# Kernel optimization log

Measured on AMD Instinct MI355X. Metric: run time of the kernel, lower is better.

Reference implementation:

```python
import jax, jax.numpy as jnp
import numpy as np

NUM_CLUSTERS = 32
EPS = 1e-12

def _l2norm(v, axis):
    return v / jnp.maximum(jnp.linalg.norm(v, axis=axis, keepdims=True), EPS)

def setup_inputs() -> dict:
    key = jax.random.key(0)
    k1, k2, k3 = jax.random.split(key, 3)
    B, M, D, K = 64, 512, 2048, NUM_CLUSTERS
    init_sc = 1.0 / np.sqrt(D)
    x = jax.random.normal(k1, (B, M, D), dtype=jnp.float32)
    W = init_sc * jax.random.normal(k2, (K, D), dtype=jnp.float32)
    centroids = init_sc * jax.random.normal(k3, (K, D), dtype=jnp.float32)
    return {"x": x, "W": W, "centroids": centroids}

def reference(x, W, centroids):
    # x: [B, M, D] frame features; W: [K, D]; centroids: [K, D]
    xn = _l2norm(x, axis=-1)                              # per-frame L2 normalize
    sa = jax.nn.softmax(jnp.einsum('bmd,kd->bmk', xn, W), axis=-1)  # [B, M, K]
    # vlad[b,k,d] = sum_m sa[b,m,k] * (xn[b,m,d] - centroids[k,d])
    #            = (sa^T @ xn)[b,k,d] - colsum(sa)[b,k] * centroids[k,d]
    agg = jnp.einsum('bmk,bmd->bkd', sa, xn)              # [B, K, D]
    vlad = agg - jnp.sum(sa, axis=1)[..., None] * centroids[None]
    vlad = _l2norm(vlad, axis=2)                          # intra-normalize per cluster
    vlad = vlad.reshape(vlad.shape[0], -1)                # [B, K*D]
    return _l2norm(vlad, axis=1)
```

## Files before the change

### kernel.cpp

```cpp
#include <hip/hip_runtime.h>
#include <hip/hip_bf16.h>
#include <cstdint>
#include <cstddef>

#define Bn 64
#define Mn 512
#define Dn 2048
#define Kn 32
#define EPSF 1e-12f

typedef __attribute__((ext_vector_type(8))) __bf16 bf16x8;
typedef __attribute__((ext_vector_type(4))) __bf16 bf16x4;
typedef __attribute__((ext_vector_type(4))) float f32x4;

__global__ __launch_bounds__(256) void k0_prep(const float* __restrict__ W,
                                               __bf16* __restrict__ Wb,
                                               float* __restrict__ colsum,
                                               float* __restrict__ ssq) {
  int idx = blockIdx.x * 256 + threadIdx.x;
  if (idx < Kn * Dn) Wb[idx] = (__bf16)W[idx];
  if (idx < Bn * Kn) { colsum[idx] = 0.f; ssq[idx] = 0.f; }
}

__global__ __launch_bounds__(256) void k1_logits_softmax(const float* __restrict__ x,
                                                         const __bf16* __restrict__ Wb,
                                                         __bf16* __restrict__ saT,
                                                         float* __restrict__ colsum) {
  int wv = threadIdx.x >> 6, lane = threadIdx.x & 63;
  int mr = lane & 15, q = lane >> 4;
  int row0 = (blockIdx.x * 4 + wv) * 16;
  int b = row0 >> 9;
  const float* xp = x + (size_t)(row0 + mr) * Dn + q * 8;
  const __bf16* wp = Wb + (size_t)mr * Dn + q * 8;
  f32x4 acc0 = {0.f, 0.f, 0.f, 0.f};
  f32x4 acc1 = {0.f, 0.f, 0.f, 0.f};
  float ssq = 0.f;
#pragma unroll 2
  for (int s = 0; s < 64; ++s) {
    f32x4 xa = *(const f32x4*)(xp + s * 32);
    f32x4 xb = *(const f32x4*)(xp + s * 32 + 4);
    bf16x8 af;
    af[0] = (__bf16)xa[0]; af[1] = (__bf16)xa[1];
    af[2] = (__bf16)xa[2]; af[3] = (__bf16)xa[3];
    af[4] = (__bf16)xb[0]; af[5] = (__bf16)xb[1];
    af[6] = (__bf16)xb[2]; af[7] = (__bf16)xb[3];
    ssq = fmaf(xa[0], xa[0], ssq); ssq = fmaf(xa[1], xa[1], ssq);
    ssq = fmaf(xa[2], xa[2], ssq); ssq = fmaf(xa[3], xa[3], ssq);
    ssq = fmaf(xb[0], xb[0], ssq); ssq = fmaf(xb[1], xb[1], ssq);
    ssq = fmaf(xb[2], xb[2], ssq); ssq = fmaf(xb[3], xb[3], ssq);
    bf16x8 b0 = *(const bf16x8*)(wp + s * 32);
    bf16x8 b1 = *(const bf16x8*)(wp + (size_t)16 * Dn + s * 32);
    acc0 = __builtin_amdgcn_mfma_f32_16x16x32_bf16(af, b0, acc0, 0, 0, 0);
    acc1 = __builtin_amdgcn_mfma_f32_16x16x32_bf16(af, b1, acc1, 0, 0, 0);
  }
  ssq += __shfl_xor(ssq, 16);
  ssq += __shfl_xor(ssq, 32);
  float invb = 1.f / fmaxf(sqrtf(ssq), EPSF);
  float cs0 = 0.f, cs1 = 0.f;
  bf16x4 v40, v41;
#pragma unroll
  for (int r = 0; r < 4; ++r) {
    float inv = __shfl(invb, q * 4 + r);
    float v0 = acc0[r] * inv, v1 = acc1[r] * inv;
    float mx = fmaxf(v0, v1);
    mx = fmaxf(mx, __shfl_xor(mx, 1));
    mx = fmaxf(mx, __shfl_xor(mx, 2));
    mx = fmaxf(mx, __shfl_xor(mx, 4));
    mx = fmaxf(mx, __shfl_xor(mx, 8));
    float e0 = __expf(v0 - mx), e1 = __expf(v1 - mx);
    float sm = e0 + e1;
    sm += __shfl_xor(sm, 1); sm += __shfl_xor(sm, 2);
    sm += __shfl_xor(sm, 4); sm += __shfl_xor(sm, 8);
    float rs = 1.f / sm;
    float sa0 = e0 * rs, sa1 = e1 * rs;
    v40[r] = (__bf16)(sa0 * inv);
    v41[r] = (__bf16)(sa1 * inv);
    cs0 += sa0; cs1 += sa1;
  }
  int mloc = row0 & 511;
  __bf16* st = saT + ((size_t)(b * Kn + mr)) * Mn + mloc + q * 4;
  *(bf16x4*)st = v40;
  *(bf16x4*)(st + (size_t)16 * Mn) = v41;
  cs0 += __shfl_xor(cs0, 16); cs0 += __shfl_xor(cs0, 32);
  cs1 += __shfl_xor(cs1, 16); cs1 += __shfl_xor(cs1, 32);
  if (lane < 16) {
    atomicAdd(&colsum[b * Kn + mr], cs0);
    atomicAdd(&colsum[b * Kn + mr + 16], cs1);
  }
}

#define AS 520
__global__ __launch_bounds__(256) void k3_agg(const float* __restrict__ x,
                                              const __bf16* __restrict__ saT,
                                              const float* __restrict__ colsum,
                                              const float* __restrict__ cent,
                                              float* __restrict__ vlad,
                                              float* __restrict__ ssq) {
  __shared__ __bf16 sal[Kn * AS];
  __shared__ float csl[Kn];
  int b = blockIdx.x >> 4;
  int dchunk = (blockIdx.x & 15) * 128;
  int t = threadIdx.x;
  const __bf16* sg = saT + (size_t)b * Kn * Mn;
#pragma unroll
  for (int i = 0; i < 8; ++i) {
    int u = t + 256 * i;
    int kr = u >> 6, off = (u & 63) * 8;
    *(bf16x8*)&sal[kr * AS + off] = *(const bf16x8*)(sg + (size_t)kr * Mn + off);
  }
  if (t < Kn) csl[t] = colsum[b * Kn + t];
  __syncthreads();
  int w = t >> 6, lane = t & 63;
  int n = lane & 15, q = lane >> 4;
  int d0 = dchunk + w * 32;
  const float* xg = x + (size_t)b * Mn * Dn;
  f32x4 acc[2][2] = {};
  for (int m0 = 0; m0 < Mn; m0 += 32) {
    bf16x8 a0 = *(const bf16x8*)&sal[n * AS + m0 + q * 8];
    bf16x8 a1 = *(const bf16x8*)&sal[(n + 16) * AS + m0 + q * 8];
#pragma unroll
    for (int dt = 0; dt < 2; ++dt) {
      const float* xp = xg + (size_t)(m0 + q * 8) * Dn + d0 + dt * 16 + n;
      bf16x8 bv;
#pragma unroll
      for (int j = 0; j < 8; ++j) bv[j] = (__bf16)xp[(size_t)j * Dn];
      acc[dt][0] = __builtin_amdgcn_mfma_f32_16x16x32_bf16(a0, bv, acc[dt][0], 0, 0, 0);
      acc[dt][1] = __builtin_amdgcn_mfma_f32_16x16x32_bf16(a1, bv, acc[dt][1], 0, 0, 0);
    }
  }
#pragma unroll
  for (int dt = 0; dt < 2; ++dt) {
#pragma unroll
    for (int kt = 0; kt < 2; ++kt) {
#pragma unroll
      for (int r = 0; r < 4; ++r) {
        int k = kt * 16 + q * 4 + r;
        int d = d0 + dt * 16 + n;
        float vv = acc[dt][kt][r] - csl[k] * cent[(size_t)k * Dn + d];
        vlad[((size_t)(b * Kn + k)) * Dn + d] = vv;
        float sq = vv * vv;
        sq += __shfl_xor(sq, 1); sq += __shfl_xor(sq, 2);
        sq += __shfl_xor(sq, 4); sq += __shfl_xor(sq, 8);
        if (n == 0) atomicAdd(&ssq[b * Kn + k], sq);
      }
    }
  }
}

__global__ __launch_bounds__(256) void k4_norm(float* __restrict__ out,
                                               const float* __restrict__ ssq) {
  __shared__ float rk[Kn];
  __shared__ float us[Kn];
  int b = blockIdx.x >> 4;
  int t = threadIdx.x;
  if (t < Kn) {
    float ss = ssq[b * Kn + t];
    float r = 1.f / fmaxf(sqrtf(ss), EPSF);
    rk[t] = r;
    us[t] = ss * r * r;
  }
  __syncthreads();
  float S = 0.f;
#pragma unroll
  for (int k = 0; k < Kn; ++k) S += us[k];
  float s = 1.f / fmaxf(sqrtf(S), EPSF);
  int chunk = blockIdx.x & 15;
  size_t base = (size_t)b * (Kn * Dn) + (size_t)chunk * 4096;
  f32x4* p = (f32x4*)(out + base);
#pragma unroll
  for (int i = 0; i < 4; ++i) {
    int idx = t + 256 * i;
    int k = (chunk * 4096 + idx * 4) >> 11;
    f32x4 v = p[idx];
    float sc = rk[k] * s;
    v[0] *= sc; v[1] *= sc; v[2] *= sc; v[3] *= sc;
    p[idx] = v;
  }
}

extern "C" void kernel_launch(void* const* d_in, const int* in_sizes, int n_in,
                              void* d_out, int out_size, void* d_ws, size_t ws_size,
                              hipStream_t stream) {
  const float* x = (const float*)d_in[0];
  const float* W = (const float*)d_in[1];
  const float* cent = (const float*)d_in[2];
  float* out = (float*)d_out;
  char* ws = (char*)d_ws;
  __bf16* Wb = (__bf16*)ws;
  float* colsum = (float*)(ws + 131072);
  float* ssqb = (float*)(ws + 131072 + 8192);
  __bf16* saT = (__bf16*)(ws + 131072 + 16384);
  hipLaunchKernelGGL(k0_prep, dim3(256), dim3(256), 0, stream, W, Wb, colsum, ssqb);
  hipLaunchKernelGGL(k1_logits_softmax, dim3(512), dim3(256), 0, stream, x, Wb, saT, colsum);
  hipLaunchKernelGGL(k3_agg, dim3(1024), dim3(256), 0, stream, x, saT, colsum, cent, out, ssqb);
  hipLaunchKernelGGL(k4_norm, dim3(1024), dim3(256), 0, stream, out, ssqb);
}
```

Baseline: 447.8 us.

## Drop W prep kernel, convert W inline, reverse k1 block order for L2 reuse

Removes the separate prep kernel that converted W to bf16 and zeroed the accumulators. W is now read as fp32 and converted inside the logits kernel, and the accumulators are zeroed with hipMemsetAsync. The logits kernel also walks its blocks in reverse, so the last-touched x rows (batch 0 region) are processed last... actually the highest batches first, so the aggregation kernel, which starts at batch 0, may find its x rows still in cache. This saves one launch but doubles W load traffic per block and adds conversion ALU work in the hot loop.

```diff
diff --git a/kernel.cpp b/kernel.cpp
--- a/kernel.cpp
+++ b/kernel.cpp
@@ -13,25 +13,18 @@
 typedef __attribute__((ext_vector_type(4))) __bf16 bf16x4;
 typedef __attribute__((ext_vector_type(4))) float f32x4;
 
-__global__ __launch_bounds__(256) void k0_prep(const float* __restrict__ W,
-                                               __bf16* __restrict__ Wb,
-                                               float* __restrict__ colsum,
-                                               float* __restrict__ ssq) {
-  int idx = blockIdx.x * 256 + threadIdx.x;
-  if (idx < Kn * Dn) Wb[idx] = (__bf16)W[idx];
-  if (idx < Bn * Kn) { colsum[idx] = 0.f; ssq[idx] = 0.f; }
-}
-
 __global__ __launch_bounds__(256) void k1_logits_softmax(const float* __restrict__ x,
-                                                         const __bf16* __restrict__ Wb,
+                                                         const float* __restrict__ W,
                                                          __bf16* __restrict__ saT,
                                                          float* __restrict__ colsum) {
   int wv = threadIdx.x >> 6, lane = threadIdx.x & 63;
   int mr = lane & 15, q = lane >> 4;
-  int row0 = (blockIdx.x * 4 + wv) * 16;
+  int blk = 511 - blockIdx.x;
+  int row0 = (blk * 4 + wv) * 16;
   int b = row0 >> 9;
   const float* xp = x + (size_t)(row0 + mr) * Dn + q * 8;
-  const __bf16* wp = Wb + (size_t)mr * Dn + q * 8;
+  const float* wp0 = W + (size_t)mr * Dn + q * 8;
+  const float* wp1 = W + (size_t)(mr + 16) * Dn + q * 8;
   f32x4 acc0 = {0.f, 0.f, 0.f, 0.f};
   f32x4 acc1 = {0.f, 0.f, 0.f, 0.f};
   float ssq = 0.f;
@@ -48,8 +41,20 @@
     ssq = fmaf(xa[2], xa[2], ssq); ssq = fmaf(xa[3], xa[3], ssq);
     ssq = fmaf(xb[0], xb[0], ssq); ssq = fmaf(xb[1], xb[1], ssq);
     ssq = fmaf(xb[2], xb[2], ssq); ssq = fmaf(xb[3], xb[3], ssq);
-    bf16x8 b0 = *(const bf16x8*)(wp + s * 32);
-    bf16x8 b1 = *(const bf16x8*)(wp + (size_t)16 * Dn + s * 32);
+    f32x4 wa = *(const f32x4*)(wp0 + s * 32);
+    f32x4 wb = *(const f32x4*)(wp0 + s * 32 + 4);
+    bf16x8 b0;
+    b0[0] = (__bf16)wa[0]; b0[1] = (__bf16)wa[1];
+    b0[2] = (__bf16)wa[2]; b0[3] = (__bf16)wa[3];
+    b0[4] = (__bf16)wb[0]; b0[5] = (__bf16)wb[1];
+    b0[6] = (__bf16)wb[2]; b0[7] = (__bf16)wb[3];
+    f32x4 wc = *(const f32x4*)(wp1 + s * 32);
+    f32x4 wd = *(const f32x4*)(wp1 + s * 32 + 4);
+    bf16x8 b1;
+    b1[0] = (__bf16)wc[0]; b1[1] = (__bf16)wc[1];
+    b1[2] = (__bf16)wc[2]; b1[3] = (__bf16)wc[3];
+    b1[4] = (__bf16)wd[0]; b1[5] = (__bf16)wd[1];
+    b1[6] = (__bf16)wd[2]; b1[7] = (__bf16)wd[3];
     acc0 = __builtin_amdgcn_mfma_f32_16x16x32_bf16(af, b0, acc0, 0, 0, 0);
     acc1 = __builtin_amdgcn_mfma_f32_16x16x32_bf16(af, b1, acc1, 0, 0, 0);
   }
@@ -186,12 +191,11 @@
   const float* cent = (const float*)d_in[2];
   float* out = (float*)d_out;
   char* ws = (char*)d_ws;
-  __bf16* Wb = (__bf16*)ws;
-  float* colsum = (float*)(ws + 131072);
-  float* ssqb = (float*)(ws + 131072 + 8192);
-  __bf16* saT = (__bf16*)(ws + 131072 + 16384);
-  hipLaunchKernelGGL(k0_prep, dim3(256), dim3(256), 0, stream, W, Wb, colsum, ssqb);
-  hipLaunchKernelGGL(k1_logits_softmax, dim3(512), dim3(256), 0, stream, x, Wb, saT, colsum);
+  float* colsum = (float*)ws;
+  float* ssqb = (float*)(ws + 8192);
+  __bf16* saT = (__bf16*)(ws + 16384);
+  hipMemsetAsync(ws, 0, 16384, stream);
+  hipLaunchKernelGGL(k1_logits_softmax, dim3(512), dim3(256), 0, stream, x, W, saT, colsum);
   hipLaunchKernelGGL(k3_agg, dim3(1024), dim3(256), 0, stream, x, saT, colsum, cent, out, ssqb);
   hipLaunchKernelGGL(k4_norm, dim3(1024), dim3(256), 0, stream, out, ssqb);
 }
```

Measured after the change: 438.9 us. 1.02x faster.
